# Optimization experiments

Measured on AMD Instinct MI355X. Metric: run time of the kernel, lower is better.

## Reference

```python
import jax, jax.numpy as jnp
import numpy as np

NUM_EXPERT = 16
IN_FEAT = 2048
OUT_FEAT = 8192
TOTAL_TOKENS = 8192


def _make_counts(rng, num_expert, total):
    # random partition of `total` tokens into `num_expert` contiguous groups
    cuts = np.sort(rng.integers(0, total + 1, size=num_expert - 1))
    counts = np.diff(np.concatenate([[0], cuts, [total]]))
    return counts.astype(np.int64)


def setup_inputs() -> dict:
    key = jax.random.key(0)
    k_inp, k_w = jax.random.split(key)
    inp = jax.random.normal(k_inp, (TOTAL_TOKENS, IN_FEAT), dtype=jnp.float32)
    # kaiming-uniform style init matching reset_parameters (fan_in = IN_FEAT)
    bound = np.sqrt(3.0) * (np.sqrt(2.0 / (1.0 + 5.0)) / np.sqrt(IN_FEAT))
    weight = jax.random.uniform(
        k_w, (NUM_EXPERT, OUT_FEAT, IN_FEAT), dtype=jnp.float32,
        minval=-bound, maxval=bound)
    rng = np.random.default_rng(0)
    fwd_expert_count = jnp.asarray(_make_counts(rng, NUM_EXPERT, TOTAL_TOKENS))
    return {"inp": inp, "weight": weight, "fwd_expert_count": fwd_expert_count}


def reference(inp, weight, fwd_expert_count):
    # Grouped GEMM: tokens are laid out contiguously per expert; group e of
    # size fwd_expert_count[e] is multiplied by weight[e]^T ([out,in] -> x@W^T).
    # fwd_expert_count is routing metadata (host-side int constants in FastMoE),
    # so slice bounds are static Python ints.
    counts = np.asarray(fwd_expert_count)
    offsets = np.concatenate([[0], np.cumsum(counts)])
    outs = []
    for e in range(weight.shape[0]):  # small fixed expert loop
        n = int(counts[e])
        seg = jax.lax.dynamic_slice_in_dim(inp, int(offsets[e]), n, axis=0)
        outs.append(jnp.einsum('ti,oi->to', seg, weight[e]))
    return jnp.concatenate(outs, axis=0)  # [total_tokens, out_feat]
```

## Files before the change

### kernel.cpp

```cpp
#include <hip/hip_runtime.h>
#include <stdint.h>
#include <stddef.h>

#define NUM_EXPERT 16
#define IN_FEAT 2048
#define OUT_FEAT 8192
#define TOTAL_TOKENS 8192

#define BM 128
#define BN 128
#define BK 32
#define KSTEPS (IN_FEAT / BK)
#define MAX_SLOTS 80

typedef __attribute__((ext_vector_type(8))) short short8;
typedef __attribute__((ext_vector_type(4))) float floatx4;
typedef __attribute__((ext_vector_type(4))) uint32_t uintx4;

__device__ __forceinline__ uint32_t pk_bf16(float a, float b) {
    uint32_t ua = __float_as_uint(a) + 0x8000u;
    uint32_t ub = __float_as_uint(b) + 0x8000u;
    return __builtin_amdgcn_perm(ub, ua, 0x07060302u);
}

__device__ __forceinline__ void cp16_to_lds(const void* g, void* l) {
    __builtin_amdgcn_global_load_lds(
        (const __attribute__((address_space(1))) uint32_t*)g,
        (__attribute__((address_space(3))) uint32_t*)l, 16, 0, 0);
}

__global__ __launch_bounds__(256) void cvt_a_kernel(const float* __restrict__ inp,
                                                    uint16_t* __restrict__ dst) {
    size_t base = ((size_t)blockIdx.x * 256 + threadIdx.x) * 8;
    floatx4 f0 = ((const floatx4*)(inp + base))[0];
    floatx4 f1 = ((const floatx4*)(inp + base))[1];
    uintx4 d;
    d.x = pk_bf16(f0.x, f0.y);
    d.y = pk_bf16(f0.z, f0.w);
    d.z = pk_bf16(f1.x, f1.y);
    d.w = pk_bf16(f1.z, f1.w);
    *(uintx4*)(dst + base) = d;
}

template <bool A_IN_WS>
__global__ __launch_bounds__(256)
void moe_gemm(const float* __restrict__ W,
              const float* __restrict__ inp,
              const uint16_t* __restrict__ Abf,
              const int* __restrict__ cnt_raw,
              float* __restrict__ out) {
    const int nt = blockIdx.x;
    const int slot = blockIdx.y;

    int sum32 = 0;
#pragma unroll
    for (int i = 0; i < NUM_EXPERT; ++i) sum32 += cnt_raw[i];
    const int idxmul = (sum32 == TOTAL_TOKENS) ? 1 : 2;

    int e = -1, lt = 0, cnt = 0, row0 = 0;
    {
        int off = 0, tacc = 0;
#pragma unroll
        for (int i = 0; i < NUM_EXPERT; ++i) {
            int c = cnt_raw[i * idxmul];
            int t = (c + BM - 1) >> 7;
            if (e < 0 && slot < tacc + t) {
                e = i; lt = slot - tacc; cnt = c; row0 = off + lt * BM;
            }
            tacc += t; off += c;
        }
    }
    if (e < 0) return;

    const int tid = threadIdx.x;
    const int lane = tid & 63;
    const int w = tid >> 6;
    const int wm = w >> 1;
    const int wn = w & 1;
    const int l15 = lane & 15;
    const int l4 = lane >> 4;

    __shared__ uint16_t Abuf[BM * BK];
    __shared__ uint16_t Bbuf[BN * BK];

    const int bn = tid >> 1;
    const int bp = (tid & 1) * 2;
    const float* bg = W + ((size_t)e * OUT_FEAT + (size_t)nt * BN + bn) * IN_FEAT + bp * 8;
    uintx4* bl0 = (uintx4*)(Bbuf + ((size_t)(bp)     * BN + bn) * 8);
    uintx4* bl1 = (uintx4*)(Bbuf + ((size_t)(bp + 1) * BN + bn) * 8);

    const uint16_t* ag0 = nullptr; const uint16_t* ag1 = nullptr;
    uint16_t* al0 = nullptr; uint16_t* al1 = nullptr;
    const float* ia = nullptr; uintx4* ial0 = nullptr; uintx4* ial1 = nullptr;
    if constexpr (A_IN_WS) {
        int c0 = tid, c1 = 256 + tid;
        int r0 = c0 >> 2, p0 = c0 & 3;
        int r1 = c1 >> 2, p1 = c1 & 3;
        int gr0 = min(row0 + r0, TOTAL_TOKENS - 1);
        int gr1 = min(row0 + r1, TOTAL_TOKENS - 1);
        ag0 = Abf + (size_t)gr0 * IN_FEAT + p0 * 8;
        ag1 = Abf + (size_t)gr1 * IN_FEAT + p1 * 8;
        al0 = Abuf + (size_t)(w * 64) * 8;
        al1 = Abuf + (size_t)(256 + w * 64) * 8;
    } else {
        int ar = tid >> 1;
        int ap = (tid & 1) * 2;
        int gr = min(row0 + ar, TOTAL_TOKENS - 1);
        ia = inp + (size_t)gr * IN_FEAT + ap * 8;
        ial0 = (uintx4*)(Abuf + (size_t)(ar * 4 + ap) * 8);
        ial1 = (uintx4*)(Abuf + (size_t)(ar * 4 + ap + 1) * 8);
    }

    const short8* Ach = (const short8*)Abuf;
    const short8* Bch = (const short8*)Bbuf;
    int aidx[4], bidx[4];
#pragma unroll
    for (int i = 0; i < 4; ++i) aidx[i] = ((wm * 64 + i * 16 + l15) << 2) + l4;
#pragma unroll
    for (int j = 0; j < 4; ++j) bidx[j] = (l4 << 7) + (wn * 64 + j * 16 + l15);

    floatx4 acc[4][4] = {};

    for (int ks = 0; ks < KSTEPS; ++ks) {
        floatx4 f0 = ((const floatx4*)bg)[0];
        floatx4 f1 = ((const floatx4*)bg)[1];
        floatx4 f2 = ((const floatx4*)bg)[2];
        floatx4 f3 = ((const floatx4*)bg)[3];
        floatx4 g0 = {}, g1 = {}, g2 = {}, g3 = {};
        if constexpr (!A_IN_WS) {
            g0 = ((const floatx4*)ia)[0];
            g1 = ((const floatx4*)ia)[1];
            g2 = ((const floatx4*)ia)[2];
            g3 = ((const floatx4*)ia)[3];
        }

        __syncthreads();

        if constexpr (A_IN_WS) {
            cp16_to_lds(ag0, al0);
            cp16_to_lds(ag1, al1);
            ag0 += BK; ag1 += BK;
        } else {
            uintx4 da0, da1;
            da0.x = pk_bf16(g0.x, g0.y); da0.y = pk_bf16(g0.z, g0.w);
            da0.z = pk_bf16(g1.x, g1.y); da0.w = pk_bf16(g1.z, g1.w);
            da1.x = pk_bf16(g2.x, g2.y); da1.y = pk_bf16(g2.z, g2.w);
            da1.z = pk_bf16(g3.x, g3.y); da1.w = pk_bf16(g3.z, g3.w);
            *ial0 = da0; *ial1 = da1;
            ia += BK;
        }
        {
            uintx4 d0, d1;
            d0.x = pk_bf16(f0.x, f0.y); d0.y = pk_bf16(f0.z, f0.w);
            d0.z = pk_bf16(f1.x, f1.y); d0.w = pk_bf16(f1.z, f1.w);
            d1.x = pk_bf16(f2.x, f2.y); d1.y = pk_bf16(f2.z, f2.w);
            d1.z = pk_bf16(f3.x, f3.y); d1.w = pk_bf16(f3.z, f3.w);
            *bl0 = d0; *bl1 = d1;
        }
        bg += BK;

        __syncthreads();

        short8 av[4], bv[4];
#pragma unroll
        for (int i = 0; i < 4; ++i) av[i] = Ach[aidx[i]];
#pragma unroll
        for (int j = 0; j < 4; ++j) bv[j] = Bch[bidx[j]];
#pragma unroll
        for (int i = 0; i < 4; ++i)
#pragma unroll
            for (int j = 0; j < 4; ++j)
                acc[i][j] = __builtin_amdgcn_mfma_f32_16x16x32_bf16(av[i], bv[j], acc[i][j], 0, 0, 0);
    }

    const int cnt_loc = cnt - lt * BM;
    const size_t col = (size_t)nt * BN + wn * 64 + l15;
#pragma unroll
    for (int i = 0; i < 4; ++i) {
        int rb = wm * 64 + i * 16 + l4 * 4;
#pragma unroll
        for (int reg = 0; reg < 4; ++reg) {
            int r = rb + reg;
            if (r < cnt_loc) {
                float* rp = out + (size_t)(row0 + r) * OUT_FEAT + col;
                rp[0]  = acc[i][0][reg];
                rp[16] = acc[i][1][reg];
                rp[32] = acc[i][2][reg];
                rp[48] = acc[i][3][reg];
            }
        }
    }
}

extern "C" void kernel_launch(void* const* d_in, const int* in_sizes, int n_in,
                              void* d_out, int out_size, void* d_ws, size_t ws_size,
                              hipStream_t stream) {
    const float* inp = (const float*)d_in[0];
    const float* W = (const float*)d_in[1];
    const int* counts = (const int*)d_in[2];
    float* out = (float*)d_out;

    const size_t abytes = (size_t)TOTAL_TOKENS * IN_FEAT * sizeof(uint16_t);
    dim3 grid(OUT_FEAT / BN, MAX_SLOTS);

    if (ws_size >= abytes) {
        uint16_t* Abf = (uint16_t*)d_ws;
        int nblk = (int)(((size_t)TOTAL_TOKENS * IN_FEAT) / (256 * 8));
        cvt_a_kernel<<<nblk, 256, 0, stream>>>(inp, Abf);
        moe_gemm<true><<<grid, 256, 0, stream>>>(W, inp, Abf, counts, out);
    } else {
        moe_gemm<false><<<grid, 256, 0, stream>>>(W, inp, nullptr, counts, out);
    }
}
```

Baseline: 1.927 ms.

## Double-buffer LDS, enlarge M tile to 256 with 512 threads, remap workgroups for XCDs

Raises the token tile to 256 rows and the workgroup to 512 threads (8 waves in a 4x2 layout), so each weight tile is converted and reused across twice as many tokens. Adds double-buffered LDS with a prologue and epilogue, so the next K-slice's global loads and conversion overlap the current MFMAs and each step needs only one barrier. The grid is flattened and blocks are remapped round-robin over 8 XCDs for better cache locality. The cost is more LDS and register pressure per workgroup, and more wasted rows in partially filled expert tiles.

```diff
diff --git a/kernel.cpp b/kernel.cpp
--- a/kernel.cpp
+++ b/kernel.cpp
@@ -7,11 +7,12 @@
 #define OUT_FEAT 8192
 #define TOTAL_TOKENS 8192
 
-#define BM 128
+#define BM 256
 #define BN 128
 #define BK 32
 #define KSTEPS (IN_FEAT / BK)
-#define MAX_SLOTS 80
+#define NT_TILES (OUT_FEAT / BN)
+#define MAX_SLOTS 48
 
 typedef __attribute__((ext_vector_type(8))) short short8;
 typedef __attribute__((ext_vector_type(4))) float floatx4;
@@ -43,14 +44,17 @@
 }
 
 template <bool A_IN_WS>
-__global__ __launch_bounds__(256)
+__global__ __launch_bounds__(512, 4)
 void moe_gemm(const float* __restrict__ W,
               const float* __restrict__ inp,
               const uint16_t* __restrict__ Abf,
               const int* __restrict__ cnt_raw,
               float* __restrict__ out) {
-    const int nt = blockIdx.x;
-    const int slot = blockIdx.y;
+    const int nwg = (int)gridDim.x;
+    const int orig = (int)blockIdx.x;
+    const int wgid = (orig & 7) * (nwg >> 3) + (orig >> 3);
+    const int slot = wgid % MAX_SLOTS;
+    const int nt = wgid / MAX_SLOTS;
 
     int sum32 = 0;
 #pragma unroll
@@ -63,7 +67,7 @@
 #pragma unroll
         for (int i = 0; i < NUM_EXPERT; ++i) {
             int c = cnt_raw[i * idxmul];
-            int t = (c + BM - 1) >> 7;
+            int t = (c + BM - 1) >> 8;
             if (e < 0 && slot < tacc + t) {
                 e = i; lt = slot - tacc; cnt = c; row0 = off + lt * BM;
             }
@@ -72,100 +76,140 @@
     }
     if (e < 0) return;
 
-    const int tid = threadIdx.x;
+    const int tid = (int)threadIdx.x;
     const int lane = tid & 63;
     const int w = tid >> 6;
-    const int wm = w >> 1;
-    const int wn = w & 1;
+    const int wm = w & 3;
+    const int wn = w >> 2;
     const int l15 = lane & 15;
     const int l4 = lane >> 4;
 
-    __shared__ uint16_t Abuf[BM * BK];
-    __shared__ uint16_t Bbuf[BN * BK];
-
-    const int bn = tid >> 1;
-    const int bp = (tid & 1) * 2;
-    const float* bg = W + ((size_t)e * OUT_FEAT + (size_t)nt * BN + bn) * IN_FEAT + bp * 8;
-    uintx4* bl0 = (uintx4*)(Bbuf + ((size_t)(bp)     * BN + bn) * 8);
-    uintx4* bl1 = (uintx4*)(Bbuf + ((size_t)(bp + 1) * BN + bn) * 8);
+    __shared__ uint16_t Abuf[2][BM * BK];
+    __shared__ uint16_t Bbuf[2][BN * BK];
+
+    const int bn_ = tid & (BN - 1);
+    const int bp_ = tid >> 7;
+    const float* bg = W + ((size_t)e * OUT_FEAT + (size_t)nt * BN + bn_) * IN_FEAT + bp_ * 8;
+    const int boff = (bp_ * BN + bn_) * 8;
 
     const uint16_t* ag0 = nullptr; const uint16_t* ag1 = nullptr;
-    uint16_t* al0 = nullptr; uint16_t* al1 = nullptr;
-    const float* ia = nullptr; uintx4* ial0 = nullptr; uintx4* ial1 = nullptr;
+    int aoff0 = 0, aoff1 = 0;
+    const float* ia = nullptr;
+    int foff0 = 0, foff1 = 0;
     if constexpr (A_IN_WS) {
-        int c0 = tid, c1 = 256 + tid;
-        int r0 = c0 >> 2, p0 = c0 & 3;
-        int r1 = c1 >> 2, p1 = c1 & 3;
+        int c0 = tid, c1 = 512 + tid;
+        int r0 = c0 & 255, p0 = c0 >> 8;
+        int r1 = c1 & 255, p1 = c1 >> 8;
         int gr0 = min(row0 + r0, TOTAL_TOKENS - 1);
         int gr1 = min(row0 + r1, TOTAL_TOKENS - 1);
         ag0 = Abf + (size_t)gr0 * IN_FEAT + p0 * 8;
         ag1 = Abf + (size_t)gr1 * IN_FEAT + p1 * 8;
-        al0 = Abuf + (size_t)(w * 64) * 8;
-        al1 = Abuf + (size_t)(256 + w * 64) * 8;
+        aoff0 = (w * 64) * 8;
+        aoff1 = (512 + w * 64) * 8;
     } else {
-        int ar = tid >> 1;
-        int ap = (tid & 1) * 2;
-        int gr = min(row0 + ar, TOTAL_TOKENS - 1);
-        ia = inp + (size_t)gr * IN_FEAT + ap * 8;
-        ial0 = (uintx4*)(Abuf + (size_t)(ar * 4 + ap) * 8);
-        ial1 = (uintx4*)(Abuf + (size_t)(ar * 4 + ap + 1) * 8);
-    }
-
-    const short8* Ach = (const short8*)Abuf;
-    const short8* Bch = (const short8*)Bbuf;
+        int r = tid & 255;
+        int pb = (tid >> 8) * 2;
+        int gr = min(row0 + r, TOTAL_TOKENS - 1);
+        ia = inp + (size_t)gr * IN_FEAT + pb * 8;
+        foff0 = (pb * 256 + r) * 8;
+        foff1 = ((pb + 1) * 256 + r) * 8;
+    }
+
     int aidx[4], bidx[4];
 #pragma unroll
-    for (int i = 0; i < 4; ++i) aidx[i] = ((wm * 64 + i * 16 + l15) << 2) + l4;
-#pragma unroll
-    for (int j = 0; j < 4; ++j) bidx[j] = (l4 << 7) + (wn * 64 + j * 16 + l15);
+    for (int i = 0; i < 4; ++i) aidx[i] = l4 * 256 + wm * 64 + i * 16 + l15;
+#pragma unroll
+    for (int j = 0; j < 4; ++j) bidx[j] = l4 * 128 + wn * 64 + j * 16 + l15;
 
     floatx4 acc[4][4] = {};
 
-    for (int ks = 0; ks < KSTEPS; ++ks) {
-        floatx4 f0 = ((const floatx4*)bg)[0];
-        floatx4 f1 = ((const floatx4*)bg)[1];
-        floatx4 f2 = ((const floatx4*)bg)[2];
-        floatx4 f3 = ((const floatx4*)bg)[3];
-        floatx4 g0 = {}, g1 = {}, g2 = {}, g3 = {};
-        if constexpr (!A_IN_WS) {
-            g0 = ((const floatx4*)ia)[0];
-            g1 = ((const floatx4*)ia)[1];
-            g2 = ((const floatx4*)ia)[2];
-            g3 = ((const floatx4*)ia)[3];
-        }
-
-        __syncthreads();
-
+    {
+        floatx4 b0 = ((const floatx4*)bg)[0];
+        floatx4 b1 = ((const floatx4*)bg)[1];
         if constexpr (A_IN_WS) {
-            cp16_to_lds(ag0, al0);
-            cp16_to_lds(ag1, al1);
+            cp16_to_lds(ag0, Abuf[0] + aoff0);
+            cp16_to_lds(ag1, Abuf[0] + aoff1);
             ag0 += BK; ag1 += BK;
         } else {
+            floatx4 a0 = ((const floatx4*)ia)[0];
+            floatx4 a1 = ((const floatx4*)ia)[1];
+            floatx4 a2 = ((const floatx4*)ia)[2];
+            floatx4 a3 = ((const floatx4*)ia)[3];
             uintx4 da0, da1;
-            da0.x = pk_bf16(g0.x, g0.y); da0.y = pk_bf16(g0.z, g0.w);
-            da0.z = pk_bf16(g1.x, g1.y); da0.w = pk_bf16(g1.z, g1.w);
-            da1.x = pk_bf16(g2.x, g2.y); da1.y = pk_bf16(g2.z, g2.w);
-            da1.z = pk_bf16(g3.x, g3.y); da1.w = pk_bf16(g3.z, g3.w);
-            *ial0 = da0; *ial1 = da1;
+            da0.x = pk_bf16(a0.x, a0.y); da0.y = pk_bf16(a0.z, a0.w);
+            da0.z = pk_bf16(a1.x, a1.y); da0.w = pk_bf16(a1.z, a1.w);
+            da1.x = pk_bf16(a2.x, a2.y); da1.y = pk_bf16(a2.z, a2.w);
+            da1.z = pk_bf16(a3.x, a3.y); da1.w = pk_bf16(a3.z, a3.w);
+            *(uintx4*)(Abuf[0] + foff0) = da0;
+            *(uintx4*)(Abuf[0] + foff1) = da1;
             ia += BK;
         }
+        uintx4 db;
+        db.x = pk_bf16(b0.x, b0.y); db.y = pk_bf16(b0.z, b0.w);
+        db.z = pk_bf16(b1.x, b1.y); db.w = pk_bf16(b1.z, b1.w);
+        *(uintx4*)(Bbuf[0] + boff) = db;
+        bg += BK;
+        __syncthreads();
+    }
+
+    for (int ks = 0; ks < KSTEPS - 1; ++ks) {
+        const int cur = ks & 1, nxt = cur ^ 1;
+
+        floatx4 b0 = ((const floatx4*)bg)[0];
+        floatx4 b1 = ((const floatx4*)bg)[1];
+        floatx4 a0, a1, a2, a3;
+        if constexpr (A_IN_WS) {
+            cp16_to_lds(ag0, Abuf[nxt] + aoff0);
+            cp16_to_lds(ag1, Abuf[nxt] + aoff1);
+            ag0 += BK; ag1 += BK;
+        } else {
+            a0 = ((const floatx4*)ia)[0];
+            a1 = ((const floatx4*)ia)[1];
+            a2 = ((const floatx4*)ia)[2];
+            a3 = ((const floatx4*)ia)[3];
+            ia += BK;
+        }
+        bg += BK;
+
+        const short8* Ach = (const short8*)Abuf[cur];
+        const short8* Bch = (const short8*)Bbuf[cur];
+        short8 av[4], bv[4];
+#pragma unroll
+        for (int j = 0; j < 4; ++j) bv[j] = Bch[bidx[j]];
+#pragma unroll
+        for (int i = 0; i < 4; ++i) av[i] = Ach[aidx[i]];
+#pragma unroll
+        for (int i = 0; i < 4; ++i)
+#pragma unroll
+            for (int j = 0; j < 4; ++j)
+                acc[i][j] = __builtin_amdgcn_mfma_f32_16x16x32_bf16(av[i], bv[j], acc[i][j], 0, 0, 0);
+
+        if constexpr (!A_IN_WS) {
+            uintx4 da0, da1;
+            da0.x = pk_bf16(a0.x, a0.y); da0.y = pk_bf16(a0.z, a0.w);
+            da0.z = pk_bf16(a1.x, a1.y); da0.w = pk_bf16(a1.z, a1.w);
+            da1.x = pk_bf16(a2.x, a2.y); da1.y = pk_bf16(a2.z, a2.w);
+            da1.z = pk_bf16(a3.x, a3.y); da1.w = pk_bf16(a3.z, a3.w);
+            *(uintx4*)(Abuf[nxt] + foff0) = da0;
+            *(uintx4*)(Abuf[nxt] + foff1) = da1;
+        }
         {
-            uintx4 d0, d1;
-            d0.x = pk_bf16(f0.x, f0.y); d0.y = pk_bf16(f0.z, f0.w);
-            d0.z = pk_bf16(f1.x, f1.y); d0.w = pk_bf16(f1.z, f1.w);
-            d1.x = pk_bf16(f2.x, f2.y); d1.y = pk_bf16(f2.z, f2.w);
-            d1.z = pk_bf16(f3.x, f3.y); d1.w = pk_bf16(f3.z, f3.w);
-            *bl0 = d0; *bl1 = d1;
-        }
-        bg += BK;
-
+            uintx4 db;
+            db.x = pk_bf16(b0.x, b0.y); db.y = pk_bf16(b0.z, b0.w);
+            db.z = pk_bf16(b1.x, b1.y); db.w = pk_bf16(b1.z, b1.w);
+            *(uintx4*)(Bbuf[nxt] + boff) = db;
+        }
         __syncthreads();
-
+    }
+
+    {
+        const short8* Ach = (const short8*)Abuf[1];
+        const short8* Bch = (const short8*)Bbuf[1];
         short8 av[4], bv[4];
 #pragma unroll
+        for (int j = 0; j < 4; ++j) bv[j] = Bch[bidx[j]];
+#pragma unroll
         for (int i = 0; i < 4; ++i) av[i] = Ach[aidx[i]];
-#pragma unroll
-        for (int j = 0; j < 4; ++j) bv[j] = Bch[bidx[j]];
 #pragma unroll
         for (int i = 0; i < 4; ++i)
 #pragma unroll
@@ -201,14 +245,14 @@
     float* out = (float*)d_out;
 
     const size_t abytes = (size_t)TOTAL_TOKENS * IN_FEAT * sizeof(uint16_t);
-    dim3 grid(OUT_FEAT / BN, MAX_SLOTS);
+    dim3 grid(NT_TILES * MAX_SLOTS);
 
     if (ws_size >= abytes) {
         uint16_t* Abf = (uint16_t*)d_ws;
         int nblk = (int)(((size_t)TOTAL_TOKENS * IN_FEAT) / (256 * 8));
         cvt_a_kernel<<<nblk, 256, 0, stream>>>(inp, Abf);
-        moe_gemm<true><<<grid, 256, 0, stream>>>(W, inp, Abf, counts, out);
+        moe_gemm<true><<<grid, 512, 0, stream>>>(W, inp, Abf, counts, out);
     } else {
-        moe_gemm<false><<<grid, 256, 0, stream>>>(W, inp, nullptr, counts, out);
-    }
-}
+        moe_gemm<false><<<grid, 512, 0, stream>>>(W, inp, nullptr, counts, out);
+    }
+}
```

After: 2.161 ms. 1.12x slower.
